# Kernel tuning notes

Measured on AMD Instinct MI355X. Metric: run time of the kernel, lower is better.

## Reference

```python
import jax, jax.numpy as jnp
import numpy as np

E = 512
H = 8
D = E // H  # head_dims = 64
MAXREL = 512


def setup_inputs() -> dict:
    key = jax.random.key(0)
    ks = jax.random.split(key, 12)
    B, L = 4, 1024
    s_lin = float(np.sqrt(6.0 / (D + D)))  # xavier uniform for (D,D)
    s_fc = float(np.sqrt(6.0 / (E + E)))
    s_tab = float(np.sqrt(6.0 / (2 * MAXREL + 1 + D)))
    return {
        "query": jax.random.normal(ks[0], (B, L, E), jnp.float32),
        "key": jax.random.normal(ks[1], (B, L, E), jnp.float32),
        "value": jax.random.normal(ks[2], (B, L, E), jnp.float32),
        "mask": jax.random.randint(ks[3], (B, 1, 1, L), 0, 2, jnp.int32),
        "Wq": jax.random.uniform(ks[4], (D, D), jnp.float32, -s_lin, s_lin),
        "bq": jnp.zeros((D,), jnp.float32),
        "Wk": jax.random.uniform(ks[5], (D, D), jnp.float32, -s_lin, s_lin),
        "bk": jnp.zeros((D,), jnp.float32),
        "Wv": jax.random.uniform(ks[6], (D, D), jnp.float32, -s_lin, s_lin),
        "bv": jnp.zeros((D,), jnp.float32),
        "Wfc": jax.random.uniform(ks[7], (E, E), jnp.float32, -s_fc, s_fc),
        "bfc": jnp.zeros((E,), jnp.float32),
        "rel_k_table": jax.random.uniform(ks[8], (2 * MAXREL + 1, D), jnp.float32, -s_tab, s_tab),
        "rel_v_table": jax.random.uniform(ks[9], (2 * MAXREL + 1, D), jnp.float32, -s_tab, s_tab),
    }


def _rel_indices(length_q, length_k):
    dist = jnp.arange(length_k)[None, :] - jnp.arange(length_q)[:, None]
    return jnp.clip(dist, -MAXREL, MAXREL) + MAXREL  # [Q, K]


def reference(query, key, value, mask, Wq, bq, Wk, bk, Wv, bv, Wfc, bfc, rel_k_table, rel_v_table):
    B, Q, _ = query.shape
    K = key.shape[1]
    q = query.reshape(B, Q, H, D) @ Wq.T + bq  # per-head linear (same weights all heads)
    k = key.reshape(B, K, H, D) @ Wk.T + bk
    v = value.reshape(B, K, H, D) @ Wv.T + bv

    scores = jnp.einsum("bqhd,bkhd->bhqk", q, k)  # [B,H,Q,K]
    scores = jnp.where(mask == 0, jnp.float32(-1e20), scores)  # mask BEFORE bias & scale, as in source

    idx = _rel_indices(Q, K)
    a_key = rel_k_table[idx]    # [Q,K,D]
    a_val = rel_v_table[idx]    # [Q,K,D]
    scores = scores + jnp.einsum("bqhd,qkd->bhqk", q, a_key)

    attn = jax.nn.softmax(scores / jnp.sqrt(jnp.float32(D)), axis=-1)

    out = jnp.einsum("bhqk,bkhd->bqhd", attn, v)  # standard AV
    out = out + jnp.einsum("bhqk,qkd->bqhd", attn, a_val)  # relative-position value term
    out = out.reshape(B, Q, H * D)
    return out @ Wfc.T + bfc
```

## Files before the change

### kernel.cpp

```cpp
#include <hip/hip_runtime.h>
#include <math.h>

#define BB 4
#define LL 1024
#define EE 512
#define HH 8
#define DD 64
#define MAXREL 512

typedef unsigned short u16;
typedef __attribute__((ext_vector_type(8))) short bf16x8;
typedef __attribute__((ext_vector_type(4))) float f32x4;
typedef __attribute__((ext_vector_type(16))) float f32x16;

__device__ __forceinline__ u16 f2bf(float f) {
    unsigned int u = __float_as_uint(f);
    unsigned int r = (u + 0x7FFFu + ((u >> 16) & 1u)) >> 16;
    return (u16)r;
}
__device__ __forceinline__ bf16x8 ldf8_bf(const float* p) {
    const float4 a = *(const float4*)(p);
    const float4 b = *(const float4*)(p + 4);
    bf16x8 r;
    r[0] = (short)f2bf(a.x); r[1] = (short)f2bf(a.y);
    r[2] = (short)f2bf(a.z); r[3] = (short)f2bf(a.w);
    r[4] = (short)f2bf(b.x); r[5] = (short)f2bf(b.y);
    r[6] = (short)f2bf(b.z); r[7] = (short)f2bf(b.w);
    return r;
}

#define MF(A, B, C)   __builtin_amdgcn_mfma_f32_16x16x32_bf16((A), (B), (C), 0, 0, 0)
#define MF32(A, B, C) __builtin_amdgcn_mfma_f32_32x32x16_bf16((A), (B), (C), 0, 0, 0)
#define EXPSC 0.1803368801111244f

__global__ __launch_bounds__(256) void proj_mfma_kernel(
    const float* __restrict__ q_in, const float* __restrict__ k_in, const float* __restrict__ v_in,
    const float* __restrict__ Wq, const float* __restrict__ bq,
    const float* __restrict__ Wk, const float* __restrict__ bk,
    const float* __restrict__ Wv, const float* __restrict__ bv,
    u16* __restrict__ qb, u16* __restrict__ kb, u16* __restrict__ vtb)
{
    int bh = blockIdx.x; int b = bh >> 3; int h = bh & 7;
    int l0 = blockIdx.y * 64;
    int t = threadIdx.x; int w = t >> 6; int lane = t & 63;
    int lg = lane >> 4, lc = lane & 15;
    int lt = l0 + w * 16;

    bf16x8 wq[4][2], wk[4][2], wv[4][2];
    #pragma unroll
    for (int dt = 0; dt < 4; ++dt)
        #pragma unroll
        for (int kc = 0; kc < 2; ++kc) {
            int d = dt * 16 + lc, ko = kc * 32 + lg * 8;
            wq[dt][kc] = ldf8_bf(Wq + d * DD + ko);
            wk[dt][kc] = ldf8_bf(Wk + d * DD + ko);
            wv[dt][kc] = ldf8_bf(Wv + d * DD + ko);
        }
    size_t xrow = ((size_t)b * LL + lt + lc) * EE + h * DD;
    bf16x8 xq[2], xk[2], xv[2];
    #pragma unroll
    for (int kc = 0; kc < 2; ++kc) {
        int ko = kc * 32 + lg * 8;
        xq[kc] = ldf8_bf(q_in + xrow + ko);
        xk[kc] = ldf8_bf(k_in + xrow + ko);
        xv[kc] = ldf8_bf(v_in + xrow + ko);
    }

    f32x4 aq[4] = {}, ak[4] = {}, av[4] = {};
    #pragma unroll
    for (int dt = 0; dt < 4; ++dt) {
        aq[dt] = MF(wq[dt][0], xq[0], aq[dt]);
        aq[dt] = MF(wq[dt][1], xq[1], aq[dt]);
        ak[dt] = MF(wk[dt][0], xk[0], ak[dt]);
        ak[dt] = MF(wk[dt][1], xk[1], ak[dt]);
        av[dt] = MF(xv[0], wv[dt][0], av[dt]);
        av[dt] = MF(xv[1], wv[dt][1], av[dt]);
    }

    #pragma unroll
    for (int dt = 0; dt < 4; ++dt) {
        u16 tq[4], tk[4], tv[4];
        #pragma unroll
        for (int r = 0; r < 4; ++r) {
            int d = dt * 16 + lg * 4 + r;
            tq[r] = f2bf(aq[dt][r] + bq[d]);
            tk[r] = f2bf(ak[dt][r] + bk[d]);
            tv[r] = f2bf(av[dt][r] + bv[dt * 16 + lc]);
        }
        size_t o = ((size_t)bh * LL + lt + lc) * DD + dt * 16 + lg * 4;
        *(uint2*)&qb[o] = *(uint2*)tq;
        *(uint2*)&kb[o] = *(uint2*)tk;
        size_t ov = ((size_t)bh * DD + dt * 16 + lc) * LL + lt + lg * 4;
        *(uint2*)&vtb[ov] = *(uint2*)tv;
    }
}

__global__ __launch_bounds__(256) void prep_kernel(
    const float* __restrict__ relk, const float* __restrict__ relv, const float* __restrict__ Wfc,
    u16* __restrict__ relk_pad, u16* __restrict__ relvt2, u16* __restrict__ wfcb)
{
    int idx = blockIdx.x * 256 + threadIdx.x;
    if (idx < 2048 * DD) {
        int r = idx >> 6, d = idx & 63;
        int j = r - 512; j = j < 0 ? 0 : (j > 2 * MAXREL ? 2 * MAXREL : j);
        relk_pad[idx] = f2bf(relk[j * DD + d]);
    }
    if (idx < DD * 3072) {
        int d = idx / 3072;
        int c = idx - d * 3072;
        int j = c - 512; j = j < 0 ? 0 : (j > 2 * MAXREL ? 2 * MAXREL : j);
        relvt2[idx] = f2bf(relv[j * DD + d]);
    }
    if (idx < EE * EE) wfcb[idx] = f2bf(Wfc[idx]);
}

__global__ __launch_bounds__(256) void attn_mfma_kernel(
    const u16* __restrict__ qb, const u16* __restrict__ kb, const u16* __restrict__ vtb,
    const int* __restrict__ mask,
    const u16* __restrict__ relk_pad, const u16* __restrict__ relvt2,
    u16* __restrict__ attn_out)
{
    __shared__ __align__(16) char smem[45312];
    u16* Ks   = (u16*)(smem);
    u16* Vts  = (u16*)(smem + 9216);
    u16* RVts = (u16*)(smem + 18432);
    u16* Ps   = (u16*)(smem + 33792);
    u16* Pqs  = (u16*)(smem + 38400);
    float* lred = (float*)(smem + 45056);
    float* obuf = (float*)smem;

    int bh = blockIdx.x, b = bh >> 3, h = bh & 7;
    int q0 = blockIdx.y * 32;
    int t = threadIdx.x, lane = t & 63, w = t >> 6;
    int rw = w & 1, cw = w >> 1;
    int rbase = rw * 16, c0a = cw * 32;
    int lg = lane >> 4, lc = lane & 15;
    int ub = c0a - rbase + 16;
    int m_ = lane & 31, h8 = (lane >> 5) * 8, hh = (lane >> 5) * 4;
    size_t bhL = (size_t)bh * LL;
    const u16* kb_bh = kb + bhL * DD;
    const u16* vt_bh = vtb + (size_t)bh * DD * LL;
    const int* mk_b = mask + b * LL;

    int sr0 = t >> 3, ss0 = (t & 7) * 8;
    int sr1 = sr0 + 32;
    int rv_row = t >> 2, rv_q = (t & 3) * 24;
    const u16* rvg = relvt2 + (size_t)rv_row * 3072 + rv_q;
    u16* rvl = RVts + rv_row * 120 + rv_q;
    const u16* rk_base = relk_pad + (size_t)(ub + lc) * DD + lg * 8;

    const u16* qrow = qb + (bhL + q0 + rbase + lc) * DD;
    bf16x8 qf0 = *(const bf16x8*)&qrow[lg * 8];
    bf16x8 qf1 = *(const bf16x8*)&qrow[32 + lg * 8];

    f32x4 s0, s1, g0, g1, g2;
    bf16x8 rk0, rk1, rk2, rk3, rk4, rk5;
    bf16x8 pa0, pa1, pr0, pr1, pr2;
    f32x16 oacc = {};
    float lacc[4] = {0.f, 0.f, 0.f, 0.f};
    int delta0 = lc - lg * 4;

#define LOAD_RK(SB) do { \
    const u16* rkp_ = rk_base + (size_t)(SB) * DD; \
    rk0 = *(const bf16x8*)&rkp_[0]; \
    rk1 = *(const bf16x8*)&rkp_[32]; \
    rk2 = *(const bf16x8*)&rkp_[16 * DD]; \
    rk3 = *(const bf16x8*)&rkp_[16 * DD + 32]; \
    rk4 = *(const bf16x8*)&rkp_[32 * DD]; \
    rk5 = *(const bf16x8*)&rkp_[32 * DD + 32]; \
} while (0)

#define DO_SCORES() do { \
    const u16* kp0_ = Ks + (c0a + lc) * 72; \
    const u16* kp1_ = Ks + (c0a + 16 + lc) * 72; \
    s0 = (f32x4){0.f,0.f,0.f,0.f}; s1 = s0; g0 = s0; g1 = s0; g2 = s0; \
    __builtin_amdgcn_s_setprio(1); \
    s0 = MF(qf0, *(const bf16x8*)&kp0_[lg * 8], s0); \
    s0 = MF(qf1, *(const bf16x8*)&kp0_[32 + lg * 8], s0); \
    s1 = MF(qf0, *(const bf16x8*)&kp1_[lg * 8], s1); \
    s1 = MF(qf1, *(const bf16x8*)&kp1_[32 + lg * 8], s1); \
    g0 = MF(qf0, rk0, g0); g0 = MF(qf1, rk1, g0); \
    g1 = MF(qf0, rk2, g1); g1 = MF(qf1, rk3, g1); \
    g2 = MF(qf0, rk4, g2); g2 = MF(qf1, rk5, g2); \
    __builtin_amdgcn_s_setprio(0); \
} while (0)

#define DO_SOFTMAX(MB0, MB1) do { \
    _Pragma("unroll") \
    for (int r = 0; r < 4; ++r) { \
        int d_ = delta0 - r; \
        int src_ = (lane & 48) | (d_ & 15); \
        float a0_ = __shfl(g0[r], src_, 64); \
        float a1_ = __shfl(g1[r], src_, 64); \
        float a2_ = __shfl(g2[r], src_, 64); \
        float gv0_ = (d_ >= 0) ? a1_ : a0_; \
        float gv1_ = (d_ >= 0) ? a2_ : a1_; \
        float p0_ = exp2f((s0[r] + (MB0) + gv0_) * EXPSC); \
        float p1_ = exp2f((s1[r] + (MB1) + gv1_) * EXPSC); \
        unsigned pk_; \
        asm("v_cvt_pk_bf16_f32 %0, %1, %2" : "=v"(pk_) : "v"(p0_), "v"(p1_)); \
        u16 pb0_ = (u16)pk_, pb1_ = (u16)(pk_ >> 16); \
        lacc[r] += p0_ + p1_; \
        int row_ = rbase + lg * 4 + r; \
        Ps[row_ * 72 + c0a + lc] = pb0_; \
        Ps[row_ * 72 + c0a + 16 + lc] = pb1_; \
        Pqs[row_ * 104 + c0a + lc - row_ + 32] = pb0_; \
        Pqs[row_ * 104 + c0a + 16 + lc - row_ + 32] = pb1_; \
    } \
} while (0)

#define READ_PFRAGS() do { \
    pa0 = *(const bf16x8*)&Ps[m_ * 72 + rw * 32 + h8]; \
    pa1 = *(const bf16x8*)&Ps[m_ * 72 + rw * 32 + 16 + h8]; \
    pr0 = *(const bf16x8*)&Pqs[m_ * 104 + rw * 48 + h8]; \
    pr1 = *(const bf16x8*)&Pqs[m_ * 104 + rw * 48 + 16 + h8]; \
    pr2 = *(const bf16x8*)&Pqs[m_ * 104 + rw * 48 + 32 + h8]; \
} while (0)

    for (int i = t; i < 416; i += 256) ((uint4*)Pqs)[i] = make_uint4(0, 0, 0, 0);
    int sb0 = 992 - q0;
    *(uint4*)&Ks[sr0 * 72 + ss0] = *(const uint4*)&kb_bh[(size_t)sr0 * DD + ss0];
    *(uint4*)&Ks[sr1 * 72 + ss0] = *(const uint4*)&kb_bh[(size_t)sr1 * DD + ss0];
    *(uint4*)&Vts[sr0 * 72 + ss0] = *(const uint4*)&vt_bh[(size_t)sr0 * LL + ss0];
    *(uint4*)&Vts[sr1 * 72 + ss0] = *(const uint4*)&vt_bh[(size_t)sr1 * LL + ss0];
    *(uint4*)&rvl[0]  = *(const uint4*)&rvg[sb0];
    *(uint4*)&rvl[8]  = *(const uint4*)&rvg[sb0 + 8];
    *(uint4*)&rvl[16] = *(const uint4*)&rvg[sb0 + 16];
    LOAD_RK(sb0);
    float mbp0 = (mk_b[c0a + lc] != 0) ? 0.f : -1e20f;
    float mbp1 = (mk_b[c0a + 16 + lc] != 0) ? 0.f : -1e20f;
    __syncthreads();
    DO_SCORES();
    LOAD_RK(sb0 + 64);
    DO_SOFTMAX(mbp0, mbp1);
    {
        uint4 k1a = *(const uint4*)&kb_bh[(size_t)(64 + sr0) * DD + ss0];
        uint4 k1b = *(const uint4*)&kb_bh[(size_t)(64 + sr1) * DD + ss0];
        __syncthreads();
        *(uint4*)&Ks[sr0 * 72 + ss0] = k1a;
        *(uint4*)&Ks[sr1 * 72 + ss0] = k1b;
        READ_PFRAGS();
        __syncthreads();
    }

    #pragma unroll 1
    for (int c = 0; c < 16; ++c) {
        int k0 = c * 64;
        int sb_ = k0 - q0 + 992;
        uint4 rK0, rK1, rV0, rV1, rRV0, rRV1, rRV2;
        float mbn0 = 0.f, mbn1 = 0.f;
        if (c < 14) {
            rK0 = *(const uint4*)&kb_bh[(size_t)(k0 + 128 + sr0) * DD + ss0];
            rK1 = *(const uint4*)&kb_bh[(size_t)(k0 + 128 + sr1) * DD + ss0];
        }
        if (c < 15) {
            int k0n = k0 + 64;
            int sbn = sb_ + 64;
            rV0  = *(const uint4*)&vt_bh[(size_t)sr0 * LL + k0n + ss0];
            rV1  = *(const uint4*)&vt_bh[(size_t)sr1 * LL + k0n + ss0];
            rRV0 = *(const uint4*)&rvg[sbn];
            rRV1 = *(const uint4*)&rvg[sbn + 8];
            rRV2 = *(const uint4*)&rvg[sbn + 16];
            mbn0 = (mk_b[k0n + c0a + lc] != 0) ? 0.f : -1e20f;
            mbn1 = (mk_b[k0n + c0a + 16 + lc] != 0) ? 0.f : -1e20f;
        }

        if (c < 15) {
            DO_SCORES();
            if (c < 14) LOAD_RK(sb_ + 128);
        }

        __builtin_amdgcn_s_setprio(1);
        {
            const u16* vrow = &Vts[(cw * 32 + m_) * 72 + rw * 32];
            const u16* rrow = &RVts[(cw * 32 + m_) * 120 + rw * 48];
            oacc = MF32(pa0, *(const bf16x8*)&vrow[h8], oacc);
            oacc = MF32(pa1, *(const bf16x8*)&vrow[16 + h8], oacc);
            oacc = MF32(pr0, *(const bf16x8*)&rrow[h8], oacc);
            oacc = MF32(pr1, *(const bf16x8*)&rrow[16 + h8], oacc);
            oacc = MF32(pr2, *(const bf16x8*)&rrow[32 + h8], oacc);
        }
        __builtin_amdgcn_s_setprio(0);

        if (c < 15) {
            DO_SOFTMAX(mbn0, mbn1);
            __syncthreads();
            if (c < 14) {
                *(uint4*)&Ks[sr0 * 72 + ss0] = rK0;
                *(uint4*)&Ks[sr1 * 72 + ss0] = rK1;
            }
            *(uint4*)&Vts[sr0 * 72 + ss0] = rV0;
            *(uint4*)&Vts[sr1 * 72 + ss0] = rV1;
            *(uint4*)&rvl[0]  = rRV0;
            *(uint4*)&rvl[8]  = rRV1;
            *(uint4*)&rvl[16] = rRV2;
            READ_PFRAGS();
            __syncthreads();
        }
    }
#undef LOAD_RK
#undef DO_SCORES
#undef DO_SOFTMAX
#undef READ_PFRAGS

    #pragma unroll
    for (int m2 = 1; m2 <= 8; m2 <<= 1) {
        #pragma unroll
        for (int r = 0; r < 4; ++r) lacc[r] += __shfl_xor(lacc[r], m2);
    }
    __syncthreads();
    if (lc == 0) {
        #pragma unroll
        for (int r = 0; r < 4; ++r) lred[cw * 32 + rbase + lg * 4 + r] = lacc[r];
    }
    __syncthreads();
    if (rw == 1) {
        #pragma unroll
        for (int reg = 0; reg < 16; ++reg) {
            int row = (reg & 3) + 8 * (reg >> 2) + hh;
            obuf[row * 68 + cw * 32 + m_] = oacc[reg];
        }
    }
    __syncthreads();
    if (rw == 0) {
        #pragma unroll
        for (int reg = 0; reg < 16; ++reg) {
            int row = (reg & 3) + 8 * (reg >> 2) + hh;
            float v = (oacc[reg] + obuf[row * 68 + cw * 32 + m_]) / (lred[row] + lred[32 + row]);
            attn_out[((size_t)b * LL + q0 + row) * EE + h * DD + cw * 32 + m_] = f2bf(v);
        }
    }
}

__global__ __launch_bounds__(256) void fc_mfma_kernel(
    const u16* __restrict__ Xb, const u16* __restrict__ Wb,
    const float* __restrict__ bfc, float* __restrict__ out)
{
    __shared__ u16 As[128][72];
    __shared__ u16 Bs[128][72];
    int m0 = blockIdx.x * 128, n0 = blockIdx.y * 128;
    int t = threadIdx.x, lane = t & 63, w = t >> 6;
    int rw = w & 1, cw = w >> 1;
    int lg = lane >> 4, lc = lane & 15;
    f32x4 acc[4][4] = {};

    for (int kt = 0; kt < EE; kt += 64) {
        __syncthreads();
        #pragma unroll
        for (int i = 0; i < 4; ++i) {
            int unit = i * 256 + t;
            int row = unit >> 3, s = unit & 7;
            *(uint4*)&As[row][s * 8] = *(const uint4*)&Xb[(size_t)(m0 + row) * EE + kt + s * 8];
            *(uint4*)&Bs[row][s * 8] = *(const uint4*)&Wb[(size_t)(n0 + row) * EE + kt + s * 8];
        }
        __syncthreads();
        #pragma unroll
        for (int kc = 0; kc < 2; ++kc) {
            bf16x8 af[4], bf[4];
            #pragma unroll
            for (int i = 0; i < 4; ++i) {
                af[i] = *(const bf16x8*)&As[rw * 64 + i * 16 + lc][kc * 32 + lg * 8];
                bf[i] = *(const bf16x8*)&Bs[cw * 64 + i * 16 + lc][kc * 32 + lg * 8];
            }
            #pragma unroll
            for (int mi = 0; mi < 4; ++mi)
                #pragma unroll
                for (int ni = 0; ni < 4; ++ni)
                    acc[mi][ni] = MF(af[mi], bf[ni], acc[mi][ni]);
        }
    }
    #pragma unroll
    for (int mi = 0; mi < 4; ++mi) {
        #pragma unroll
        for (int ni = 0; ni < 4; ++ni) {
            int n = n0 + cw * 64 + ni * 16 + lc;
            float bias = bfc[n];
            #pragma unroll
            for (int r = 0; r < 4; ++r) {
                int m = m0 + rw * 64 + mi * 16 + lg * 4 + r;
                out[(size_t)m * EE + n] = acc[mi][ni][r] + bias;
            }
        }
    }
}

extern "C" void kernel_launch(void* const* d_in, const int* in_sizes, int n_in,
                              void* d_out, int out_size, void* d_ws, size_t ws_size,
                              hipStream_t stream) {
    const float* query = (const float*)d_in[0];
    const float* key   = (const float*)d_in[1];
    const float* value = (const float*)d_in[2];
    const int*   mask  = (const int*)d_in[3];
    const float* Wq  = (const float*)d_in[4];
    const float* bq  = (const float*)d_in[5];
    const float* Wk  = (const float*)d_in[6];
    const float* bk  = (const float*)d_in[7];
    const float* Wv  = (const float*)d_in[8];
    const float* bv  = (const float*)d_in[9];
    const float* Wfc = (const float*)d_in[10];
    const float* bfc = (const float*)d_in[11];
    const float* relk = (const float*)d_in[12];
    const float* relv = (const float*)d_in[13];
    float* out = (float*)d_out;

    char* ws = (char*)d_ws;
    u16* qb        = (u16*)(ws);
    u16* kb        = (u16*)(ws + (4u << 20));
    u16* vtb       = (u16*)(ws + (8u << 20));
    u16* attnb     = (u16*)(ws + (12u << 20));
    u16* relk_pad  = (u16*)(ws + (16u << 20));
    u16* relvt2    = (u16*)(ws + (16u << 20) + 262144);
    u16* wfcb      = (u16*)(ws + (16u << 20) + 655360);

    proj_mfma_kernel<<<dim3(BB * HH, LL / 64), 256, 0, stream>>>(
        query, key, value, Wq, bq, Wk, bk, Wv, bv, qb, kb, vtb);
    prep_kernel<<<1024, 256, 0, stream>>>(relk, relv, Wfc, relk_pad, relvt2, wfcb);
    attn_mfma_kernel<<<dim3(BB * HH, LL / 32), 256, 0, stream>>>(
        qb, kb, vtb, mask, relk_pad, relvt2, attnb);
    fc_mfma_kernel<<<dim3(BB * LL / 128, EE / 128), 256, 0, stream>>>(attnb, wfcb, bfc, out);
}
```

Measured before the change: 107.2 us.

## Fold prep into projection kernel, split AV accumulators, shrink RV smem stride

Removes the separate prep kernel launch by adding 8x16 extra blocks to the projection grid that convert the relative tables and Wfc to bf16 in parallel with the projections. In the attention kernel, the single MFMA output accumulator is split into separate V and relative-V accumulators so that consecutive MFMAs no longer depend on each other, at the cost of 16 extra registers. The relative-V LDS row stride drops from 120 to 104, which shrinks shared memory and may change bank-conflict behaviour.

```diff
diff --git a/kernel.cpp b/kernel.cpp
--- a/kernel.cpp
+++ b/kernel.cpp
@@ -38,11 +38,34 @@
     const float* __restrict__ Wq, const float* __restrict__ bq,
     const float* __restrict__ Wk, const float* __restrict__ bk,
     const float* __restrict__ Wv, const float* __restrict__ bv,
-    u16* __restrict__ qb, u16* __restrict__ kb, u16* __restrict__ vtb)
+    const float* __restrict__ relk, const float* __restrict__ relv, const float* __restrict__ Wfc,
+    u16* __restrict__ qb, u16* __restrict__ kb, u16* __restrict__ vtb,
+    u16* __restrict__ relk_pad, u16* __restrict__ relvt2, u16* __restrict__ wfcb)
 {
+    int t = threadIdx.x;
+    if (blockIdx.x >= 32) {
+        int pid = (blockIdx.x - 32) * 16 + blockIdx.y;
+        #pragma unroll
+        for (int i = 0; i < 8; ++i) {
+            int idx = pid * 256 + i * 32768 + t;
+            if (idx < 2048 * DD) {
+                int r = idx >> 6, d = idx & 63;
+                int j = r - 512; j = j < 0 ? 0 : (j > 2 * MAXREL ? 2 * MAXREL : j);
+                relk_pad[idx] = f2bf(relk[j * DD + d]);
+            }
+            if (idx < DD * 3072) {
+                int d = idx / 3072;
+                int c = idx - d * 3072;
+                int j = c - 512; j = j < 0 ? 0 : (j > 2 * MAXREL ? 2 * MAXREL : j);
+                relvt2[idx] = f2bf(relv[j * DD + d]);
+            }
+            if (idx < EE * EE) wfcb[idx] = f2bf(Wfc[idx]);
+        }
+        return;
+    }
     int bh = blockIdx.x; int b = bh >> 3; int h = bh & 7;
     int l0 = blockIdx.y * 64;
-    int t = threadIdx.x; int w = t >> 6; int lane = t & 63;
+    int w = t >> 6; int lane = t & 63;
     int lg = lane >> 4, lc = lane & 15;
     int lt = l0 + w * 16;
 
@@ -95,38 +118,19 @@
     }
 }
 
-__global__ __launch_bounds__(256) void prep_kernel(
-    const float* __restrict__ relk, const float* __restrict__ relv, const float* __restrict__ Wfc,
-    u16* __restrict__ relk_pad, u16* __restrict__ relvt2, u16* __restrict__ wfcb)
-{
-    int idx = blockIdx.x * 256 + threadIdx.x;
-    if (idx < 2048 * DD) {
-        int r = idx >> 6, d = idx & 63;
-        int j = r - 512; j = j < 0 ? 0 : (j > 2 * MAXREL ? 2 * MAXREL : j);
-        relk_pad[idx] = f2bf(relk[j * DD + d]);
-    }
-    if (idx < DD * 3072) {
-        int d = idx / 3072;
-        int c = idx - d * 3072;
-        int j = c - 512; j = j < 0 ? 0 : (j > 2 * MAXREL ? 2 * MAXREL : j);
-        relvt2[idx] = f2bf(relv[j * DD + d]);
-    }
-    if (idx < EE * EE) wfcb[idx] = f2bf(Wfc[idx]);
-}
-
 __global__ __launch_bounds__(256) void attn_mfma_kernel(
     const u16* __restrict__ qb, const u16* __restrict__ kb, const u16* __restrict__ vtb,
     const int* __restrict__ mask,
     const u16* __restrict__ relk_pad, const u16* __restrict__ relvt2,
     u16* __restrict__ attn_out)
 {
-    __shared__ __align__(16) char smem[45312];
+    __shared__ __align__(16) char smem[43264];
     u16* Ks   = (u16*)(smem);
     u16* Vts  = (u16*)(smem + 9216);
     u16* RVts = (u16*)(smem + 18432);
-    u16* Ps   = (u16*)(smem + 33792);
-    u16* Pqs  = (u16*)(smem + 38400);
-    float* lred = (float*)(smem + 45056);
+    u16* Ps   = (u16*)(smem + 31744);
+    u16* Pqs  = (u16*)(smem + 36352);
+    float* lred = (float*)(smem + 43008);
     float* obuf = (float*)smem;
 
     int bh = blockIdx.x, b = bh >> 3, h = bh & 7;
@@ -146,7 +150,7 @@
     int sr1 = sr0 + 32;
     int rv_row = t >> 2, rv_q = (t & 3) * 24;
     const u16* rvg = relvt2 + (size_t)rv_row * 3072 + rv_q;
-    u16* rvl = RVts + rv_row * 120 + rv_q;
+    u16* rvl = RVts + rv_row * 104 + rv_q;
     const u16* rk_base = relk_pad + (size_t)(ub + lc) * DD + lg * 8;
 
     const u16* qrow = qb + (bhL + q0 + rbase + lc) * DD;
@@ -156,7 +160,7 @@
     f32x4 s0, s1, g0, g1, g2;
     bf16x8 rk0, rk1, rk2, rk3, rk4, rk5;
     bf16x8 pa0, pa1, pr0, pr1, pr2;
-    f32x16 oacc = {};
+    f32x16 oaccV = {}, oaccR = {};
     float lacc[4] = {0.f, 0.f, 0.f, 0.f};
     int delta0 = lc - lg * 4;
 
@@ -273,12 +277,12 @@
         __builtin_amdgcn_s_setprio(1);
         {
             const u16* vrow = &Vts[(cw * 32 + m_) * 72 + rw * 32];
-            const u16* rrow = &RVts[(cw * 32 + m_) * 120 + rw * 48];
-            oacc = MF32(pa0, *(const bf16x8*)&vrow[h8], oacc);
-            oacc = MF32(pa1, *(const bf16x8*)&vrow[16 + h8], oacc);
-            oacc = MF32(pr0, *(const bf16x8*)&rrow[h8], oacc);
-            oacc = MF32(pr1, *(const bf16x8*)&rrow[16 + h8], oacc);
-            oacc = MF32(pr2, *(const bf16x8*)&rrow[32 + h8], oacc);
+            const u16* rrow = &RVts[(cw * 32 + m_) * 104 + rw * 48];
+            oaccV = MF32(pa0, *(const bf16x8*)&vrow[h8], oaccV);
+            oaccR = MF32(pr0, *(const bf16x8*)&rrow[h8], oaccR);
+            oaccV = MF32(pa1, *(const bf16x8*)&vrow[16 + h8], oaccV);
+            oaccR = MF32(pr1, *(const bf16x8*)&rrow[16 + h8], oaccR);
+            oaccR = MF32(pr2, *(const bf16x8*)&rrow[32 + h8], oaccR);
         }
         __builtin_amdgcn_s_setprio(0);
 
@@ -318,7 +322,7 @@
         #pragma unroll
         for (int reg = 0; reg < 16; ++reg) {
             int row = (reg & 3) + 8 * (reg >> 2) + hh;
-            obuf[row * 68 + cw * 32 + m_] = oacc[reg];
+            obuf[row * 68 + cw * 32 + m_] = oaccV[reg] + oaccR[reg];
         }
     }
     __syncthreads();
@@ -326,7 +330,7 @@
         #pragma unroll
         for (int reg = 0; reg < 16; ++reg) {
             int row = (reg & 3) + 8 * (reg >> 2) + hh;
-            float v = (oacc[reg] + obuf[row * 68 + cw * 32 + m_]) / (lred[row] + lred[32 + row]);
+            float v = (oaccV[reg] + oaccR[reg] + obuf[row * 68 + cw * 32 + m_]) / (lred[row] + lred[32 + row]);
             attn_out[((size_t)b * LL + q0 + row) * EE + h * DD + cw * 32 + m_] = f2bf(v);
         }
     }
@@ -412,9 +416,9 @@
     u16* relvt2    = (u16*)(ws + (16u << 20) + 262144);
     u16* wfcb      = (u16*)(ws + (16u << 20) + 655360);
 
-    proj_mfma_kernel<<<dim3(BB * HH, LL / 64), 256, 0, stream>>>(
-        query, key, value, Wq, bq, Wk, bk, Wv, bv, qb, kb, vtb);
-    prep_kernel<<<1024, 256, 0, stream>>>(relk, relv, Wfc, relk_pad, relvt2, wfcb);
+    proj_mfma_kernel<<<dim3(40, LL / 64), 256, 0, stream>>>(
+        query, key, value, Wq, bq, Wk, bk, Wv, bv, relk, relv, Wfc,
+        qb, kb, vtb, relk_pad, relvt2, wfcb);
     attn_mfma_kernel<<<dim3(BB * HH, LL / 32), 256, 0, stream>>>(
         qb, kb, vtb, mask, relk_pad, relvt2, attnb);
     fc_mfma_kernel<<<dim3(BB * LL / 128, EE / 128), 256, 0, stream>>>(attnb, wfcb, bfc, out);
```

Measured after the change: 109.9 us. 2.5% more time.
